# Kernel optimization log

Hardware: AMD Instinct MI355X
Metric: run time of the kernel (lower is better)

## Reference

```python
import jax, jax.numpy as jnp
import numpy as np

NEG_SLOPE = 0.01  # nn.LeakyReLU default
EM_DIM = 64

def setup_inputs() -> dict:
    key = jax.random.key(0)
    k1, k2, k3, k4, k5 = jax.random.split(key, 5)
    B, N, D = 4, 512, EM_DIM
    embeddings = jax.random.normal(k1, (B, N, D), dtype=jnp.float32)
    # att_W: Linear(D, D) -> weight [D, D], bias [D]
    W_w = jax.random.normal(k2, (D, D), dtype=jnp.float32) * (1.0 / np.sqrt(D))
    W_b = jax.random.normal(k3, (D,), dtype=jnp.float32) * 0.01
    # att_a: Linear(3D, 1) -> weight [3D], bias scalar
    a_w = jax.random.normal(k4, (3 * D,), dtype=jnp.float32) * (1.0 / np.sqrt(3 * D))
    a_b = jax.random.normal(k5, (1,), dtype=jnp.float32) * 0.01
    return {"embeddings": embeddings, "W_w": W_w, "W_b": W_b, "a_w": a_w, "a_b": a_b}

def reference(embeddings, W_w, W_b, a_w, a_b):
    # embeddings: [B, N, D]
    D = embeddings.shape[-1]
    # pairwise elementwise product: value[b,i,j,d] = e[b,i,d] * e[b,j,d]
    value = embeddings[:, :, None, :] * embeddings[:, None, :, :]  # [B,N,N,D]
    # att_W applied to (broadcast) query/key is row/col-constant -> compute once per node
    w_e = jnp.einsum('bnd,ed->bne', embeddings, W_w) + W_b   # [B,N,D] (= wq rows = wk cols)
    wv = jnp.einsum('bijd,ed->bije', value, W_w) + W_b       # [B,N,N,D]
    # att_a on concat(wq, wk, wv): split the weight vector into three D-chunks
    a_q, a_k, a_v = a_w[:D], a_w[D:2*D], a_w[2*D:]
    s_q = w_e @ a_q  # [B,N]
    s_k = w_e @ a_k  # [B,N]
    s = s_q[:, :, None] + s_k[:, None, :] + jnp.einsum('bije,e->bij', wv, a_v) + a_b[0]  # [B,N,N]
    s = jnp.where(s >= 0, s, NEG_SLOPE * s)  # LeakyReLU; dropout is identity in eval
    alphas = jax.nn.softmax(s, axis=-1)[..., None]  # [B,N,N,1]
    return alphas, value
```

## Files before the change

### kernel.cpp

```cpp
#include <hip/hip_runtime.h>

#define DD 64
#define NN 512
#define BB 4
#define NEG_SLOPE 0.01f

typedef float floatx4 __attribute__((ext_vector_type(4)));

__global__ void precompute_kernel(const float* __restrict__ W_w,
                                  const float* __restrict__ W_b,
                                  const float* __restrict__ a_w,
                                  const float* __restrict__ a_b,
                                  float* __restrict__ ws) {
    int d = threadIdx.x;
    float cq = 0.f, ck = 0.f, cv = 0.f;
    for (int e = 0; e < DD; ++e) {
        float w = W_w[e * DD + d];
        cq = fmaf(a_w[e], w, cq);
        ck = fmaf(a_w[DD + e], w, ck);
        cv = fmaf(a_w[2 * DD + e], w, cv);
    }
    ws[d] = cq;
    ws[DD + d] = ck;
    ws[2 * DD + d] = cv;
    float p = W_b[d] * (a_w[d] + a_w[DD + d] + a_w[2 * DD + d]);
#pragma unroll
    for (int off = 32; off; off >>= 1) p += __shfl_down(p, off, 64);
    if (d == 0) ws[3 * DD] = p + a_b[0];
}

__global__ __launch_bounds__(256) void fused_kernel(
        const float* __restrict__ emb,
        const float* __restrict__ ws,
        float* __restrict__ out_alpha,
        float* __restrict__ out_value) {
    const int row = blockIdx.x;
    const int b = row >> 9;
    const int t = threadIdx.x;
    const int d4 = t & 15;
    const int jl = t >> 4;

    __shared__ float s_part[NN][17];
    __shared__ float red[8];

    const floatx4* emb4 = (const floatx4*)emb;
    const floatx4 ei = emb4[(size_t)row * 16 + d4];
    const floatx4 cq = ((const floatx4*)ws)[d4];
    const floatx4 ck = ((const floatx4*)(ws + DD))[d4];
    const floatx4 cv = ((const floatx4*)(ws + 2 * DD))[d4];
    const float Cc = ws[3 * DD];

    const floatx4* embB = emb4 + (size_t)b * NN * 16;
    floatx4* val4 = (floatx4*)out_value + (size_t)row * NN * 16;

    const floatx4 cvec = ei * cv + ck;
    const float pq = ei.x * cq.x + ei.y * cq.y + ei.z * cq.z + ei.w * cq.w;

#pragma unroll 8
    for (int it = 0; it < NN / 16; ++it) {
        const int j = it * 16 + jl;
        const floatx4 ej = embB[j * 16 + d4];
        const floatx4 p = ei * ej;
        val4[j * 16 + d4] = p;
        s_part[j][d4] = ej.x * cvec.x + ej.y * cvec.y
                      + ej.z * cvec.z + ej.w * cvec.w + pq;
    }
    __syncthreads();

    float s0 = 0.f, s1 = 0.f;
#pragma unroll
    for (int k = 0; k < 16; ++k) {
        s0 += s_part[t][k];
        s1 += s_part[t + 256][k];
    }
    s0 += Cc; s1 += Cc;
    s0 = (s0 >= 0.f) ? s0 : NEG_SLOPE * s0;
    s1 = (s1 >= 0.f) ? s1 : NEG_SLOPE * s1;

    float m = fmaxf(s0, s1);
#pragma unroll
    for (int off = 32; off; off >>= 1) m = fmaxf(m, __shfl_xor(m, off, 64));
    const int wid = t >> 6, lane = t & 63;
    if (lane == 0) red[wid] = m;
    __syncthreads();
    m = fmaxf(fmaxf(red[0], red[1]), fmaxf(red[2], red[3]));

    float e0 = expf(s0 - m), e1 = expf(s1 - m);
    float ps = e0 + e1;
#pragma unroll
    for (int off = 32; off; off >>= 1) ps += __shfl_xor(ps, off, 64);
    if (lane == 0) red[4 + wid] = ps;
    __syncthreads();
    const float inv = 1.f / (red[4] + red[5] + red[6] + red[7]);

    float* arow = out_alpha + (size_t)row * NN;
    arow[t] = e0 * inv;
    arow[t + 256] = e1 * inv;
}

extern "C" void kernel_launch(void* const* d_in, const int* in_sizes, int n_in,
                              void* d_out, int out_size, void* d_ws, size_t ws_size,
                              hipStream_t stream) {
    const float* emb = (const float*)d_in[0];
    const float* W_w = (const float*)d_in[1];
    const float* W_b = (const float*)d_in[2];
    const float* a_w = (const float*)d_in[3];
    const float* a_b = (const float*)d_in[4];
    float* ws = (float*)d_ws;

    float* out = (float*)d_out;
    float* out_alpha = out;
    float* out_value = out + (size_t)BB * NN * NN;

    precompute_kernel<<<1, 64, 0, stream>>>(W_w, W_b, a_w, a_b, ws);
    fused_kernel<<<BB * NN, 256, 0, stream>>>(emb, ws, out_alpha, out_value);
}
```

Baseline: 275.4 us.

## Split value materialization into separate multi-row kernel from softmax kernel

```diff
diff --git a/kernel.cpp b/kernel.cpp
--- a/kernel.cpp
+++ b/kernel.cpp
@@ -3,6 +3,7 @@
 #define DD 64
 #define NN 512
 #define BB 4
+#define IT 4
 #define NEG_SLOPE 0.01f
 
 typedef float floatx4 __attribute__((ext_vector_type(4)));
@@ -29,11 +30,40 @@
     if (d == 0) ws[3 * DD] = p + a_b[0];
 }
 
-__global__ __launch_bounds__(256) void fused_kernel(
+__global__ __launch_bounds__(512) void value_kernel(
+        const float* __restrict__ emb,
+        float* __restrict__ out_value) {
+    const int blk = blockIdx.x;
+    const int b = blk >> 7;
+    const int i0 = (blk & 127) * IT;
+    const int t = threadIdx.x;
+    const int d4 = t & 15;
+    const int jl = t >> 4;
+
+    const floatx4* emb4 = (const floatx4*)emb;
+    const floatx4* embB = emb4 + (size_t)b * NN * 16;
+
+    floatx4 ei[IT];
+#pragma unroll
+    for (int r = 0; r < IT; ++r) ei[r] = embB[(i0 + r) * 16 + d4];
+
+    floatx4* valB = (floatx4*)out_value + ((size_t)b * NN + i0) * NN * 16;
+
+#pragma unroll 4
+    for (int jo = 0; jo < NN / 32; ++jo) {
+        const int j = jo * 32 + jl;
+        const floatx4 ej = embB[j * 16 + d4];
+#pragma unroll
+        for (int r = 0; r < IT; ++r) {
+            valB[((size_t)r * NN + j) * 16 + d4] = ei[r] * ej;
+        }
+    }
+}
+
+__global__ __launch_bounds__(256) void alpha_kernel(
         const float* __restrict__ emb,
         const float* __restrict__ ws,
-        float* __restrict__ out_alpha,
-        float* __restrict__ out_value) {
+        float* __restrict__ out_alpha) {
     const int row = blockIdx.x;
     const int b = row >> 9;
     const int t = threadIdx.x;
@@ -51,7 +81,6 @@
     const float Cc = ws[3 * DD];
 
     const floatx4* embB = emb4 + (size_t)b * NN * 16;
-    floatx4* val4 = (floatx4*)out_value + (size_t)row * NN * 16;
 
     const floatx4 cvec = ei * cv + ck;
     const float pq = ei.x * cq.x + ei.y * cq.y + ei.z * cq.z + ei.w * cq.w;
@@ -60,8 +89,6 @@
     for (int it = 0; it < NN / 16; ++it) {
         const int j = it * 16 + jl;
         const floatx4 ej = embB[j * 16 + d4];
-        const floatx4 p = ei * ej;
-        val4[j * 16 + d4] = p;
         s_part[j][d4] = ej.x * cvec.x + ej.y * cvec.y
                       + ej.z * cvec.z + ej.w * cvec.w + pq;
     }
@@ -112,6 +139,7 @@
     float* out_alpha = out;
     float* out_value = out + (size_t)BB * NN * NN;
 
+    value_kernel<<<BB * NN / IT, 512, 0, stream>>>(emb, out_value);
     precompute_kernel<<<1, 64, 0, stream>>>(W_w, W_b, a_w, a_b, ws);
-    fused_kernel<<<BB * NN, 256, 0, stream>>>(emb, ws, out_alpha, out_value);
+    alpha_kernel<<<BB * NN, 256, 0, stream>>>(emb, ws, out_alpha);
 }
```

Result: slower. 283.6 us (+3.0%).
